# Kernel optimization log

Hardware: AMD Instinct MI355X
Metric: run time of the kernel (lower is better)

## Reference

```python
import jax, jax.numpy as jnp
import numpy as np

B, H, W, C = 8, 64, 64, 64
C8 = C // 8

def setup_inputs() -> dict:
    key = jax.random.key(0)
    ks = jax.random.split(key, 5)
    x = jax.random.normal(ks[0], (B, H, W, C), dtype=jnp.float32)
    # 1x1 conv kernels (fan-in scaled) + biases
    wq = jax.random.normal(ks[1], (C, C8), dtype=jnp.float32) / np.sqrt(C)
    wk = jax.random.normal(ks[2], (C, C8), dtype=jnp.float32) / np.sqrt(C)
    wv = jax.random.normal(ks[3], (C, C), dtype=jnp.float32) / np.sqrt(C)
    bq = jnp.zeros((C8,), dtype=jnp.float32)
    bk = jnp.zeros((C8,), dtype=jnp.float32)
    bv = jnp.zeros((C,), dtype=jnp.float32)
    gamma = jax.random.normal(ks[4], (), dtype=jnp.float32)
    return {"x": x, "wq": wq, "bq": bq, "wk": wk, "bk": bk,
            "wv": wv, "bv": bv, "gamma": gamma}

def reference(x, wq, bq, wk, bk, wv, bv, gamma):
    b, h, w, c = x.shape
    n = h * w
    # 1x1 convs == per-pixel linear projections
    q = (jnp.einsum('bhwc,cd->bhwd', x, wq) + bq).reshape(b, n, -1)  # [B,N,C/8]
    k = (jnp.einsum('bhwc,cd->bhwd', x, wk) + bk).reshape(b, n, -1)  # [B,N,C/8]
    v = (jnp.einsum('bhwc,cd->bhwd', x, wv) + bv).reshape(b, n, -1)  # [B,N,C]
    # Unscaled attention: softmax over keys (last axis), no 1/sqrt(d)
    attn = jax.nn.softmax(jnp.einsum('bnd,bmd->bnm', q, k), axis=-1)  # [B,N,N]
    out = jnp.einsum('bnm,bmc->bnc', attn, v).reshape(b, h, w, c)
    return out * gamma + x
```

## Files before the change

kernel.cpp:

```cpp
#include <hip/hip_runtime.h>
#include <hip/hip_bf16.h>


#define BB 8
#define NN 4096
#define CC 64
#define PSTRIDE 72
#define LOG2E 1.44269504088896f

typedef _Float16 f16;
typedef _Float16 half8 __attribute__((ext_vector_type(8)));
typedef _Float16 half4 __attribute__((ext_vector_type(4)));
typedef __fp16 fp16x2 __attribute__((ext_vector_type(2)));
typedef float floatx4 __attribute__((ext_vector_type(4)));

static __device__ inline half4 pack4(float a, float b, float c, float d) {
    fp16x2 lo = __builtin_amdgcn_cvt_pkrtz(a, b);
    fp16x2 hi = __builtin_amdgcn_cvt_pkrtz(c, d);
    unsigned int lou = __builtin_bit_cast(unsigned int, lo);
    unsigned int hiu = __builtin_bit_cast(unsigned int, hi);
    unsigned long long packed = (unsigned long long)lou | ((unsigned long long)hiu << 32);
    return __builtin_bit_cast(half4, packed);
}


__global__ __launch_bounds__(256) void proj_all_kernel(
    const float* __restrict__ x,
    const float* __restrict__ wq, const float* __restrict__ bq,
    const float* __restrict__ wk, const float* __restrict__ bk,
    const float* __restrict__ wv, const float* __restrict__ bv,
    f16* __restrict__ Qh, f16* __restrict__ Kf, f16* __restrict__ Vf,
    float* __restrict__ qn2, float* __restrict__ kn2)
{
    __shared__ alignas(16) f16 Ws[80][PSTRIDE];
    __shared__ float Bs[80];
    __shared__ alignas(16) f16 Vs[64][68];
    __shared__ alignas(16) f16 Ks[64][12];
    const int tid = threadIdx.x;

    for (int i = tid; i < 4096; i += 256) {
        int cin = i >> 6, cout = i & 63;
        Ws[cout][cin] = (f16)wv[i];
    }
    for (int i = tid; i < 512; i += 256) {
        int cin = i >> 3, c = i & 7;
        Ws[64 + c][cin] = (f16)(wq[i] * LOG2E);
        Ws[72 + c][cin] = (f16)wk[i];
    }
    if (tid < 80)
        Bs[tid] = (tid < 64) ? bv[tid]
                : (tid < 72 ? bq[tid - 64] * LOG2E : bk[tid - 72]);
    __syncthreads();

    const int wave = tid >> 6, lane = tid & 63;
    const int quad = lane >> 4, n16 = lane & 15;
    const long pb = (long)blockIdx.x * 64;
    const long p0 = pb + wave * 16;
    const int  b   = (int)(pb >> 12);
    const int  nnb = (int)(pb & 4095);

    half8 ax[2];
#pragma unroll
    for (int kh = 0; kh < 2; ++kh) {
        const float* xp = x + (p0 + n16) * 64 + kh * 32 + quad * 8;
        float4 x1 = *(const float4*)xp;
        float4 x2 = *(const float4*)(xp + 4);
        ax[kh][0] = (f16)x1.x; ax[kh][1] = (f16)x1.y;
        ax[kh][2] = (f16)x1.z; ax[kh][3] = (f16)x1.w;
        ax[kh][4] = (f16)x2.x; ax[kh][5] = (f16)x2.y;
        ax[kh][6] = (f16)x2.z; ax[kh][7] = (f16)x2.w;
    }

#pragma unroll
    for (int ct = 0; ct < 5; ++ct) {
        const int cout = (ct < 4) ? ct * 16 + n16 : 64 + n16;
        const float bias = Bs[cout];
        half8 b0 = *(const half8*)(&Ws[cout][quad * 8]);
        half8 b1 = *(const half8*)(&Ws[cout][32 + quad * 8]);
        floatx4 acc = {bias, bias, bias, bias};
        acc = __builtin_amdgcn_mfma_f32_16x16x32_f16(ax[0], b0, acc, 0, 0, 0);
        acc = __builtin_amdgcn_mfma_f32_16x16x32_f16(ax[1], b1, acc, 0, 0, 0);
        if (ct < 4) {
#pragma unroll
            for (int r = 0; r < 4; ++r)
                Vs[wave * 16 + quad * 4 + r][ct * 16 + n16] = (f16)acc[r];
        } else {
            float n2[4];
#pragma unroll
            for (int r = 0; r < 4; ++r) n2[r] = acc[r] * acc[r];
#pragma unroll
            for (int d = 1; d < 8; d <<= 1)
#pragma unroll
                for (int r = 0; r < 4; ++r) n2[r] += __shfl_xor(n2[r], d, 64);
            if (n16 == 0) {
#pragma unroll
                for (int r = 0; r < 4; ++r) qn2[p0 + quad * 4 + r] = n2[r];
            } else if (n16 == 8) {
#pragma unroll
                for (int r = 0; r < 4; ++r) kn2[p0 + quad * 4 + r] = n2[r];
            }
            if (n16 < 8) {
                f16* dst = Qh + (p0 + quad * 4) * 8 + n16;
#pragma unroll
                for (int r = 0; r < 4; ++r) dst[r * 8] = (f16)acc[r];
            } else {
#pragma unroll
                for (int r = 0; r < 4; ++r)
                    Ks[wave * 16 + quad * 4 + r][n16 - 8] = (f16)acc[r];
            }
        }
    }
    __syncthreads();

#pragma unroll
    for (int u = 0; u < 2; ++u) {
        const int tt = wave * 2 + u;
        const int kb = tt >> 2, ct = tt & 3;
        half8 v;
#pragma unroll
        for (int j = 0; j < 8; ++j)
            v[j] = Vs[kb * 32 + quad * 8 + j][ct * 16 + n16];
        const size_t kbg = (size_t)b * 128 + (nnb >> 5) + kb;
        *(half8*)(Vf + (kbg * 4 + ct) * 512 + lane * 8) = v;
    }
    if (wave < 2) {
        half8 kp;
#pragma unroll
        for (int e = 0; e < 2; ++e) {
            const int t = wave * 2 + e;
#pragma unroll
            for (int j = 0; j < 4; ++j) {
                f16 v = (f16)0.f;
                if (quad < 2) v = Ks[t * 16 + n16][quad * 4 + j];
                else if (quad == 2 && j == 0) v = (f16)1.f;
                kp[e * 4 + j] = v;
            }
        }
        const size_t kpg = (size_t)b * 128 + (nnb >> 5) + wave;
        *(half8*)(Kf + kpg * 512 + lane * 8) = kp;
    }
}

__global__ __launch_bounds__(256) void knorm_max_kernel(
    const float* __restrict__ kn2, float* __restrict__ Mk2)
{
    __shared__ float red[4];
    const int b = blockIdx.x, tid = threadIdx.x;
    float mx = 0.f;
    for (int i = tid; i < NN; i += 256) mx = fmaxf(mx, kn2[(size_t)b * NN + i]);
#pragma unroll
    for (int d = 1; d < 64; d <<= 1) mx = fmaxf(mx, __shfl_xor(mx, d, 64));
    if ((tid & 63) == 0) red[tid >> 6] = mx;
    __syncthreads();
    if (tid == 0) Mk2[b] = fmaxf(fmaxf(red[0], red[1]), fmaxf(red[2], red[3]));
}

__global__ __launch_bounds__(256, 3) void attn_kernel(
    const f16* __restrict__ Qh, const f16* __restrict__ Kf,
    const f16* __restrict__ Vf,
    const float* __restrict__ qn2, const float* __restrict__ Mk2,
    const float* __restrict__ x, const float* __restrict__ gptr,
    float* __restrict__ out)
{
    __shared__ alignas(16) char smem[24576];
    f16*   Pbuf = (f16*)smem;
    float* Obuf = (float*)smem;
    __shared__ float Ls[4][2][16];

    const int tid  = threadIdx.x;
    const int wave = tid >> 6, lane = tid & 63;
    const int quad = lane >> 4, n16 = lane & 15;
    const int ks = wave;

    const int b  = blockIdx.x & 7;
    const int qt = blockIdx.x >> 3;
    const size_t bN = (size_t)b * NN;

    const float mk2 = Mk2[b];

    half4 bq4[2];
#pragma unroll
    for (int qt2 = 0; qt2 < 2; ++qt2) {
        const int q = qt * 32 + qt2 * 16 + n16;
        const float mf = __builtin_sqrtf(qn2[bN + q] * mk2) - 12.0f;
        half4 v = {0, 0, 0, 0};
        if (quad < 2)
            v = *(const half4*)(Qh + (bN + q) * 8 + quad * 4);
        else if (quad == 2)
            v[0] = (f16)(-mf);
        bq4[qt2] = v;
    }

    floatx4 oacc[2][4];
#pragma unroll
    for (int qt2 = 0; qt2 < 2; ++qt2)
#pragma unroll
        for (int ct = 0; ct < 4; ++ct) oacc[qt2][ct] = (floatx4){0.f, 0.f, 0.f, 0.f};
    float l_loc[2] = {0.f, 0.f};

    const f16* kfb = Kf + ((size_t)b * 128 + ks * 32) * 512;
    const f16* vfb = Vf + ((size_t)b * 128 + ks * 32) * 2048;
    const floatx4 zero4 = {0.f, 0.f, 0.f, 0.f};
    f16* Pw0 = Pbuf + (wave * 2 + 0) * 16 * PSTRIDE;
    f16* Pw1 = Pbuf + (wave * 2 + 1) * 16 * PSTRIDE;

    for (int it = 0; it < 16; ++it) {
        half8 kk0 = *(const half8*)(kfb + (size_t)(it * 2 + 0) * 512 + lane * 8);
        half8 kk1 = *(const half8*)(kfb + (size_t)(it * 2 + 1) * 512 + lane * 8);
        half8 av0[4], av1[4];
#pragma unroll
        for (int ct = 0; ct < 4; ++ct)
            av0[ct] = *(const half8*)(vfb + ((size_t)(it * 2) * 4 + ct) * 512 + lane * 8);
#pragma unroll
        for (int ct = 0; ct < 4; ++ct)
            av1[ct] = *(const half8*)(vfb + ((size_t)(it * 2 + 1) * 4 + ct) * 512 + lane * 8);

        half4 ak[4];
        ak[0] = __builtin_shufflevector(kk0, kk0, 0, 1, 2, 3);
        ak[1] = __builtin_shufflevector(kk0, kk0, 4, 5, 6, 7);
        ak[2] = __builtin_shufflevector(kk1, kk1, 0, 1, 2, 3);
        ak[3] = __builtin_shufflevector(kk1, kk1, 4, 5, 6, 7);

        floatx4 sf[4];
#pragma unroll
        for (int t = 0; t < 4; ++t)
            sf[t] = __builtin_amdgcn_mfma_f32_16x16x16f16(ak[t], bq4[0], zero4, 0, 0, 0);

#pragma unroll
        for (int qt2 = 0; qt2 < 2; ++qt2) {
            if (qt2 == 1) {
#pragma unroll
                for (int t = 0; t < 4; ++t)
                    sf[t] = __builtin_amdgcn_mfma_f32_16x16x16f16(ak[t], bq4[1], zero4, 0, 0, 0);
            }
            float rst[4];
#pragma unroll
            for (int t = 0; t < 4; ++t) {
                float pv0 = __builtin_exp2f(sf[t][0]);
                float pv1 = __builtin_exp2f(sf[t][1]);
                float pv2 = __builtin_exp2f(sf[t][2]);
                float pv3 = __builtin_exp2f(sf[t][3]);
                sf[t][0] = pv0; sf[t][1] = pv1; sf[t][2] = pv2; sf[t][3] = pv3;
                rst[t] = (pv0 + pv1) + (pv2 + pv3);
            }
            l_loc[qt2] += (rst[0] + rst[1]) + (rst[2] + rst[3]);
            f16* Pw = qt2 ? Pw1 : Pw0;
#pragma unroll
            for (int t = 0; t < 4; ++t) {
                half4 pk = pack4(sf[t][0], sf[t][1], sf[t][2], sf[t][3]);
                *(half4*)(Pw + n16 * PSTRIDE + t * 16 + quad * 4) = pk;
            }
        }
        __asm__ volatile("s_waitcnt lgkmcnt(0)" ::: "memory");

#pragma unroll
        for (int qt2 = 0; qt2 < 2; ++qt2) {
            f16* Pw = qt2 ? Pw1 : Pw0;
            half8 bp0 = *(const half8*)(Pw + n16 * PSTRIDE + quad * 8);
            half8 bp1 = *(const half8*)(Pw + n16 * PSTRIDE + 32 + quad * 8);
#pragma unroll
            for (int ct = 0; ct < 4; ++ct)
                oacc[qt2][ct] = __builtin_amdgcn_mfma_f32_16x16x32_f16(av0[ct], bp0, oacc[qt2][ct], 0, 0, 0);
#pragma unroll
            for (int ct = 0; ct < 4; ++ct)
                oacc[qt2][ct] = __builtin_amdgcn_mfma_f32_16x16x32_f16(av1[ct], bp1, oacc[qt2][ct], 0, 0, 0);
        }
    }

    float l_run[2];
#pragma unroll
    for (int qt2 = 0; qt2 < 2; ++qt2) {
        float l = l_loc[qt2];
        l += __shfl_xor(l, 16, 64);
        l += __shfl_xor(l, 32, 64);
        l_run[qt2] = l;
    }

    __syncthreads();
    if (ks > 0) {
#pragma unroll
        for (int qt2 = 0; qt2 < 2; ++qt2) {
            if (quad == 0) Ls[ks][qt2][n16] = l_run[qt2];
            float* ob = Obuf + (((ks - 1) * 2 + qt2) * 64 + lane) * 16;
#pragma unroll
            for (int ct = 0; ct < 4; ++ct)
                *(floatx4*)(ob + ct * 4) = oacc[qt2][ct];
        }
    }
    __syncthreads();
    if (ks == 0) {
        const float g = gptr[0];
#pragma unroll
        for (int qt2 = 0; qt2 < 2; ++qt2) {
            float l = l_run[qt2];
            float o[16];
#pragma unroll
            for (int ct = 0; ct < 4; ++ct)
#pragma unroll
                for (int r = 0; r < 4; ++r) o[ct * 4 + r] = oacc[qt2][ct][r];
#pragma unroll
            for (int p = 1; p < 4; ++p) {
                l += Ls[p][qt2][n16];
                const float* ob = Obuf + (((p - 1) * 2 + qt2) * 64 + lane) * 16;
#pragma unroll
                for (int i = 0; i < 16; ++i) o[i] += ob[i];
            }
            const float scale = g / l;
            const int q = qt * 32 + qt2 * 16 + n16;
#pragma unroll
            for (int ct = 0; ct < 4; ++ct) {
                const size_t idx = (bN + q) * CC + ct * 16 + quad * 4;
                float4 xr = *(const float4*)(x + idx);
                float4 res;
                res.x = o[ct * 4 + 0] * scale + xr.x;
                res.y = o[ct * 4 + 1] * scale + xr.y;
                res.z = o[ct * 4 + 2] * scale + xr.z;
                res.w = o[ct * 4 + 3] * scale + xr.w;
                *(float4*)(out + idx) = res;
            }
        }
    }
}

extern "C" void kernel_launch(void* const* d_in, const int* in_sizes, int n_in,
                              void* d_out, int out_size, void* d_ws, size_t ws_size,
                              hipStream_t stream) {
    const float* x     = (const float*)d_in[0];
    const float* wq    = (const float*)d_in[1];
    const float* bq    = (const float*)d_in[2];
    const float* wk    = (const float*)d_in[3];
    const float* bk    = (const float*)d_in[4];
    const float* wv    = (const float*)d_in[5];
    const float* bv    = (const float*)d_in[6];
    const float* gamma = (const float*)d_in[7];
    float* out = (float*)d_out;

    f16* Qh = (f16*)d_ws;
    f16* Kf = Qh + (size_t)BB * NN * 8;
    f16* Vf = Kf + (size_t)BB * 128 * 512;
    float* qn2 = (float*)(Vf + (size_t)BB * 128 * 4 * 512);
    float* kn2 = qn2 + (size_t)BB * NN;
    float* Mk2 = kn2 + (size_t)BB * NN;

    proj_all_kernel<<<512, 256, 0, stream>>>(x, wq, bq, wk, bk, wv, bv,
                                             Qh, Kf, Vf, qn2, kn2);
    knorm_max_kernel<<<BB, 256, 0, stream>>>(kn2, Mk2);
    attn_kernel<<<BB * 128, 256, 0, stream>>>(Qh, Kf, Vf, qn2, Mk2, x, gamma, out);
}
```

Measured before the change: 128.4 us.

## Software-pipeline attention loop with double-buffered P tiles and K prefetch

The attention loop becomes a software pipeline. Each iteration computes QK^T and exp for step it into one LDS P buffer while running the PV MFMAs for step it-1 from the other buffer, and K and V fragments are prefetched one step ahead. Launch bounds rise to 4 blocks per SM, shared memory grows to 36 KB, and the cross-wave output reduction buffer is padded to stride 20 and read with vector loads to cut bank conflicts. The cost is more LDS and register pressure, which may limit occupancy or force spills.

```diff
diff --git a/kernel.cpp b/kernel.cpp
--- a/kernel.cpp
+++ b/kernel.cpp
@@ -155,17 +155,17 @@
     if (tid == 0) Mk2[b] = fmaxf(fmaxf(red[0], red[1]), fmaxf(red[2], red[3]));
 }
 
-__global__ __launch_bounds__(256, 3) void attn_kernel(
+__global__ __launch_bounds__(256, 4) void attn_kernel(
     const f16* __restrict__ Qh, const f16* __restrict__ Kf,
     const f16* __restrict__ Vf,
     const float* __restrict__ qn2, const float* __restrict__ Mk2,
     const float* __restrict__ x, const float* __restrict__ gptr,
     float* __restrict__ out)
 {
-    __shared__ alignas(16) char smem[24576];
-    f16*   Pbuf = (f16*)smem;
-    float* Obuf = (float*)smem;
+    __shared__ alignas(16) char smem[36864];
     __shared__ float Ls[4][2][16];
+    f16*   Pbase = (f16*)smem;
+    float* Obuf  = (float*)smem;
 
     const int tid  = threadIdx.x;
     const int wave = tid >> 6, lane = tid & 63;
@@ -198,72 +198,136 @@
         for (int ct = 0; ct < 4; ++ct) oacc[qt2][ct] = (floatx4){0.f, 0.f, 0.f, 0.f};
     float l_loc[2] = {0.f, 0.f};
 
-    const f16* kfb = Kf + ((size_t)b * 128 + ks * 32) * 512;
-    const f16* vfb = Vf + ((size_t)b * 128 + ks * 32) * 2048;
+    const f16* kfb = Kf + ((size_t)b * 128 + ks * 32) * 512 + lane * 8;
+    const f16* vfb = Vf + ((size_t)b * 128 + ks * 32) * 2048 + lane * 8;
     const floatx4 zero4 = {0.f, 0.f, 0.f, 0.f};
-    f16* Pw0 = Pbuf + (wave * 2 + 0) * 16 * PSTRIDE;
-    f16* Pw1 = Pbuf + (wave * 2 + 1) * 16 * PSTRIDE;
-
-    for (int it = 0; it < 16; ++it) {
-        half8 kk0 = *(const half8*)(kfb + (size_t)(it * 2 + 0) * 512 + lane * 8);
-        half8 kk1 = *(const half8*)(kfb + (size_t)(it * 2 + 1) * 512 + lane * 8);
-        half8 av0[4], av1[4];
+
+    f16* PA = Pbase + wave * 2304;
+    f16* PB = Pbase + 9216 + wave * 2304;
+
+    half8 kkc0 = *(const half8*)(kfb + 0);
+    half8 kkc1 = *(const half8*)(kfb + 512);
+    half8 kkn0, kkn1;
+    half8 av0[4], av1[4];
+
+    {
+        half4 ak[4];
+        ak[0] = __builtin_shufflevector(kkc0, kkc0, 0, 1, 2, 3);
+        ak[1] = __builtin_shufflevector(kkc0, kkc0, 4, 5, 6, 7);
+        ak[2] = __builtin_shufflevector(kkc1, kkc1, 0, 1, 2, 3);
+        ak[3] = __builtin_shufflevector(kkc1, kkc1, 4, 5, 6, 7);
+
+        kkn0 = *(const half8*)(kfb + 1024);
+        kkn1 = *(const half8*)(kfb + 1536);
 #pragma unroll
         for (int ct = 0; ct < 4; ++ct)
-            av0[ct] = *(const half8*)(vfb + ((size_t)(it * 2) * 4 + ct) * 512 + lane * 8);
+            av0[ct] = *(const half8*)(vfb + (size_t)ct * 512);
 #pragma unroll
         for (int ct = 0; ct < 4; ++ct)
-            av1[ct] = *(const half8*)(vfb + ((size_t)(it * 2 + 1) * 4 + ct) * 512 + lane * 8);
+            av1[ct] = *(const half8*)(vfb + (size_t)(4 + ct) * 512);
+
+        floatx4 sf[4];
+#pragma unroll
+        for (int qt2 = 0; qt2 < 2; ++qt2) {
+#pragma unroll
+            for (int t = 0; t < 4; ++t)
+                sf[t] = __builtin_amdgcn_mfma_f32_16x16x16f16(ak[t], bq4[qt2], zero4, 0, 0, 0);
+            float rst[4];
+            f16* Pw = PA + qt2 * 1152 + n16 * PSTRIDE;
+#pragma unroll
+            for (int t = 0; t < 4; ++t) {
+                float p0 = __builtin_exp2f(sf[t][0]);
+                float p1 = __builtin_exp2f(sf[t][1]);
+                float p2 = __builtin_exp2f(sf[t][2]);
+                float p3 = __builtin_exp2f(sf[t][3]);
+                rst[t] = (p0 + p1) + (p2 + p3);
+                *(half4*)(Pw + t * 16 + quad * 4) = pack4(p0, p1, p2, p3);
+            }
+            l_loc[qt2] += (rst[0] + rst[1]) + (rst[2] + rst[3]);
+        }
+        kkc0 = kkn0; kkc1 = kkn1;
+    }
+
+    for (int it = 1; it < 16; ++it) {
+        f16* Pr = (it & 1) ? PA : PB;
+        f16* Pw = (it & 1) ? PB : PA;
+
+        __asm__ volatile("s_waitcnt lgkmcnt(0)" ::: "memory");
+        half8 bp[2][2];
+#pragma unroll
+        for (int qt2 = 0; qt2 < 2; ++qt2) {
+            const f16* p = Pr + qt2 * 1152 + n16 * PSTRIDE;
+            bp[qt2][0] = *(const half8*)(p + quad * 8);
+            bp[qt2][1] = *(const half8*)(p + 32 + quad * 8);
+        }
 
         half4 ak[4];
-        ak[0] = __builtin_shufflevector(kk0, kk0, 0, 1, 2, 3);
-        ak[1] = __builtin_shufflevector(kk0, kk0, 4, 5, 6, 7);
-        ak[2] = __builtin_shufflevector(kk1, kk1, 0, 1, 2, 3);
-        ak[3] = __builtin_shufflevector(kk1, kk1, 4, 5, 6, 7);
+        ak[0] = __builtin_shufflevector(kkc0, kkc0, 0, 1, 2, 3);
+        ak[1] = __builtin_shufflevector(kkc0, kkc0, 4, 5, 6, 7);
+        ak[2] = __builtin_shufflevector(kkc1, kkc1, 0, 1, 2, 3);
+        ak[3] = __builtin_shufflevector(kkc1, kkc1, 4, 5, 6, 7);
+
+        const int itn = (it < 15) ? it + 1 : 15;
+        kkn0 = *(const half8*)(kfb + (size_t)itn * 1024);
+        kkn1 = *(const half8*)(kfb + (size_t)itn * 1024 + 512);
 
         floatx4 sf[4];
 #pragma unroll
-        for (int t = 0; t < 4; ++t)
-            sf[t] = __builtin_amdgcn_mfma_f32_16x16x16f16(ak[t], bq4[0], zero4, 0, 0, 0);
-
-#pragma unroll
-        for (int qt2 = 0; qt2 < 2; ++qt2) {
-            if (qt2 == 1) {
-#pragma unroll
-                for (int t = 0; t < 4; ++t)
-                    sf[t] = __builtin_amdgcn_mfma_f32_16x16x16f16(ak[t], bq4[1], zero4, 0, 0, 0);
-            }
+        for (int qt2 = 0; qt2 < 2; ++qt2) {
+#pragma unroll
+            for (int t = 0; t < 4; ++t)
+                sf[t] = __builtin_amdgcn_mfma_f32_16x16x16f16(ak[t], bq4[qt2], zero4, 0, 0, 0);
             float rst[4];
+            f16* Pq = Pw + qt2 * 1152 + n16 * PSTRIDE;
 #pragma unroll
             for (int t = 0; t < 4; ++t) {
-                float pv0 = __builtin_exp2f(sf[t][0]);
-                float pv1 = __builtin_exp2f(sf[t][1]);
-                float pv2 = __builtin_exp2f(sf[t][2]);
-                float pv3 = __builtin_exp2f(sf[t][3]);
-                sf[t][0] = pv0; sf[t][1] = pv1; sf[t][2] = pv2; sf[t][3] = pv3;
-                rst[t] = (pv0 + pv1) + (pv2 + pv3);
+                float p0 = __builtin_exp2f(sf[t][0]);
+                float p1 = __builtin_exp2f(sf[t][1]);
+                float p2 = __builtin_exp2f(sf[t][2]);
+                float p3 = __builtin_exp2f(sf[t][3]);
+                rst[t] = (p0 + p1) + (p2 + p3);
+                *(half4*)(Pq + t * 16 + quad * 4) = pack4(p0, p1, p2, p3);
             }
             l_loc[qt2] += (rst[0] + rst[1]) + (rst[2] + rst[3]);
-            f16* Pw = qt2 ? Pw1 : Pw0;
-#pragma unroll
-            for (int t = 0; t < 4; ++t) {
-                half4 pk = pack4(sf[t][0], sf[t][1], sf[t][2], sf[t][3]);
-                *(half4*)(Pw + n16 * PSTRIDE + t * 16 + quad * 4) = pk;
-            }
-        }
+        }
+
+#pragma unroll
+        for (int qt2 = 0; qt2 < 2; ++qt2) {
+#pragma unroll
+            for (int ct = 0; ct < 4; ++ct)
+                oacc[qt2][ct] = __builtin_amdgcn_mfma_f32_16x16x32_f16(av0[ct], bp[qt2][0], oacc[qt2][ct], 0, 0, 0);
+#pragma unroll
+            for (int ct = 0; ct < 4; ++ct)
+                oacc[qt2][ct] = __builtin_amdgcn_mfma_f32_16x16x32_f16(av1[ct], bp[qt2][1], oacc[qt2][ct], 0, 0, 0);
+        }
+
+#pragma unroll
+        for (int ct = 0; ct < 4; ++ct)
+            av0[ct] = *(const half8*)(vfb + ((size_t)(it * 2) * 4 + ct) * 512);
+#pragma unroll
+        for (int ct = 0; ct < 4; ++ct)
+            av1[ct] = *(const half8*)(vfb + ((size_t)(it * 2 + 1) * 4 + ct) * 512);
+
+        kkc0 = kkn0; kkc1 = kkn1;
+    }
+
+    {
         __asm__ volatile("s_waitcnt lgkmcnt(0)" ::: "memory");
-
-#pragma unroll
-        for (int qt2 = 0; qt2 < 2; ++qt2) {
-            f16* Pw = qt2 ? Pw1 : Pw0;
-            half8 bp0 = *(const half8*)(Pw + n16 * PSTRIDE + quad * 8);
-            half8 bp1 = *(const half8*)(Pw + n16 * PSTRIDE + 32 + quad * 8);
-#pragma unroll
-            for (int ct = 0; ct < 4; ++ct)
-                oacc[qt2][ct] = __builtin_amdgcn_mfma_f32_16x16x32_f16(av0[ct], bp0, oacc[qt2][ct], 0, 0, 0);
-#pragma unroll
-            for (int ct = 0; ct < 4; ++ct)
-                oacc[qt2][ct] = __builtin_amdgcn_mfma_f32_16x16x32_f16(av1[ct], bp1, oacc[qt2][ct], 0, 0, 0);
+        half8 bp[2][2];
+#pragma unroll
+        for (int qt2 = 0; qt2 < 2; ++qt2) {
+            const f16* p = PB + qt2 * 1152 + n16 * PSTRIDE;
+            bp[qt2][0] = *(const half8*)(p + quad * 8);
+            bp[qt2][1] = *(const half8*)(p + 32 + quad * 8);
+        }
+#pragma unroll
+        for (int qt2 = 0; qt2 < 2; ++qt2) {
+#pragma unroll
+            for (int ct = 0; ct < 4; ++ct)
+                oacc[qt2][ct] = __builtin_amdgcn_mfma_f32_16x16x32_f16(av0[ct], bp[qt2][0], oacc[qt2][ct], 0, 0, 0);
+#pragma unroll
+            for (int ct = 0; ct < 4; ++ct)
+                oacc[qt2][ct] = __builtin_amdgcn_mfma_f32_16x16x32_f16(av1[ct], bp[qt2][1], oacc[qt2][ct], 0, 0, 0);
         }
     }
 
@@ -281,7 +345,7 @@
 #pragma unroll
         for (int qt2 = 0; qt2 < 2; ++qt2) {
             if (quad == 0) Ls[ks][qt2][n16] = l_run[qt2];
-            float* ob = Obuf + (((ks - 1) * 2 + qt2) * 64 + lane) * 16;
+            float* ob = Obuf + (size_t)(((ks - 1) * 2 + qt2) * 64 + lane) * 20;
 #pragma unroll
             for (int ct = 0; ct < 4; ++ct)
                 *(floatx4*)(ob + ct * 4) = oacc[qt2][ct];
@@ -301,9 +365,13 @@
 #pragma unroll
             for (int p = 1; p < 4; ++p) {
                 l += Ls[p][qt2][n16];
-                const float* ob = Obuf + (((p - 1) * 2 + qt2) * 64 + lane) * 16;
-#pragma unroll
-                for (int i = 0; i < 16; ++i) o[i] += ob[i];
+                const float* ob = Obuf + (size_t)(((p - 1) * 2 + qt2) * 64 + lane) * 20;
+#pragma unroll
+                for (int ct = 0; ct < 4; ++ct) {
+                    floatx4 t = *(const floatx4*)(ob + ct * 4);
+                    o[ct * 4 + 0] += t[0]; o[ct * 4 + 1] += t[1];
+                    o[ct * 4 + 2] += t[2]; o[ct * 4 + 3] += t[3];
+                }
             }
             const float scale = g / l;
             const int q = qt * 32 + qt2 * 16 + n16;
```

Result: no change. 127.4 us (-0.7%).

## Feed P directly from MFMA registers into PV MFMA, removing LDS round-trip

Applied to the files above, without the earlier changes.

The V fragment layout in the prep kernel is permuted so that the score MFMA output (16x16x16, four f16 values per lane) can be packed and fed straight into the P·V MFMA as the B operand, using 16x16x16 instructions instead of 16x16x32. This drops the per-iteration write of P to shared memory, the lgkmcnt wait and the read back. K fragments are also prefetched one iteration ahead. The reduction buffer stride is padded from 16 to 20 floats and read with vector loads to reduce bank conflicts. The cost is twice as many (smaller) MFMA instructions for the P·V product and extra registers for the prefetched K.

```diff
diff --git a/kernel.cpp b/kernel.cpp
--- a/kernel.cpp
+++ b/kernel.cpp
@@ -118,8 +118,11 @@
         const int kb = tt >> 2, ct = tt & 3;
         half8 v;
 #pragma unroll
-        for (int j = 0; j < 8; ++j)
-            v[j] = Vs[kb * 32 + quad * 8 + j][ct * 16 + n16];
+        for (int j = 0; j < 4; ++j)
+            v[j] = Vs[kb * 32 + quad * 4 + j][ct * 16 + n16];
+#pragma unroll
+        for (int j = 0; j < 4; ++j)
+            v[4 + j] = Vs[kb * 32 + 16 + quad * 4 + j][ct * 16 + n16];
         const size_t kbg = (size_t)b * 128 + (nnb >> 5) + kb;
         *(half8*)(Vf + (kbg * 4 + ct) * 512 + lane * 8) = v;
     }
@@ -162,10 +165,9 @@
     const float* __restrict__ x, const float* __restrict__ gptr,
     float* __restrict__ out)
 {
-    __shared__ alignas(16) char smem[24576];
-    f16*   Pbuf = (f16*)smem;
+    __shared__ alignas(16) char smem[30720];
+    __shared__ float Ls[4][2][16];
     float* Obuf = (float*)smem;
-    __shared__ float Ls[4][2][16];
 
     const int tid  = threadIdx.x;
     const int wave = tid >> 6, lane = tid & 63;
@@ -198,72 +200,62 @@
         for (int ct = 0; ct < 4; ++ct) oacc[qt2][ct] = (floatx4){0.f, 0.f, 0.f, 0.f};
     float l_loc[2] = {0.f, 0.f};
 
-    const f16* kfb = Kf + ((size_t)b * 128 + ks * 32) * 512;
-    const f16* vfb = Vf + ((size_t)b * 128 + ks * 32) * 2048;
+    const f16* kfb = Kf + ((size_t)b * 128 + ks * 32) * 512 + lane * 8;
+    const f16* vfb = Vf + ((size_t)b * 128 + ks * 32) * 2048 + lane * 8;
     const floatx4 zero4 = {0.f, 0.f, 0.f, 0.f};
-    f16* Pw0 = Pbuf + (wave * 2 + 0) * 16 * PSTRIDE;
-    f16* Pw1 = Pbuf + (wave * 2 + 1) * 16 * PSTRIDE;
+
+    half8 kkc0 = *(const half8*)(kfb + 0);
+    half8 kkc1 = *(const half8*)(kfb + 512);
 
     for (int it = 0; it < 16; ++it) {
-        half8 kk0 = *(const half8*)(kfb + (size_t)(it * 2 + 0) * 512 + lane * 8);
-        half8 kk1 = *(const half8*)(kfb + (size_t)(it * 2 + 1) * 512 + lane * 8);
-        half8 av0[4], av1[4];
-#pragma unroll
-        for (int ct = 0; ct < 4; ++ct)
-            av0[ct] = *(const half8*)(vfb + ((size_t)(it * 2) * 4 + ct) * 512 + lane * 8);
-#pragma unroll
-        for (int ct = 0; ct < 4; ++ct)
-            av1[ct] = *(const half8*)(vfb + ((size_t)(it * 2 + 1) * 4 + ct) * 512 + lane * 8);
+        half8 avp[2][4];
+#pragma unroll
+        for (int p = 0; p < 2; ++p)
+#pragma unroll
+            for (int ct = 0; ct < 4; ++ct)
+                avp[p][ct] = *(const half8*)(vfb + ((size_t)(it * 2 + p) * 4 + ct) * 512);
 
         half4 ak[4];
-        ak[0] = __builtin_shufflevector(kk0, kk0, 0, 1, 2, 3);
-        ak[1] = __builtin_shufflevector(kk0, kk0, 4, 5, 6, 7);
-        ak[2] = __builtin_shufflevector(kk1, kk1, 0, 1, 2, 3);
-        ak[3] = __builtin_shufflevector(kk1, kk1, 4, 5, 6, 7);
-
-        floatx4 sf[4];
-#pragma unroll
-        for (int t = 0; t < 4; ++t)
-            sf[t] = __builtin_amdgcn_mfma_f32_16x16x16f16(ak[t], bq4[0], zero4, 0, 0, 0);
+        ak[0] = __builtin_shufflevector(kkc0, kkc0, 0, 1, 2, 3);
+        ak[1] = __builtin_shufflevector(kkc0, kkc0, 4, 5, 6, 7);
+        ak[2] = __builtin_shufflevector(kkc1, kkc1, 0, 1, 2, 3);
+        ak[3] = __builtin_shufflevector(kkc1, kkc1, 4, 5, 6, 7);
+
+        const int itn = (it < 15) ? it + 1 : 15;
+        kkc0 = *(const half8*)(kfb + (size_t)itn * 1024);
+        kkc1 = *(const half8*)(kfb + (size_t)itn * 1024 + 512);
 
 #pragma unroll
         for (int qt2 = 0; qt2 < 2; ++qt2) {
-            if (qt2 == 1) {
-#pragma unroll
-                for (int t = 0; t < 4; ++t)
-                    sf[t] = __builtin_amdgcn_mfma_f32_16x16x16f16(ak[t], bq4[1], zero4, 0, 0, 0);
-            }
+            floatx4 sf[4];
+#pragma unroll
+            for (int t = 0; t < 4; ++t)
+                sf[t] = __builtin_amdgcn_mfma_f32_16x16x16f16(ak[t], bq4[qt2], zero4, 0, 0, 0);
+
+            half4 pk[4];
             float rst[4];
 #pragma unroll
             for (int t = 0; t < 4; ++t) {
-                float pv0 = __builtin_exp2f(sf[t][0]);
-                float pv1 = __builtin_exp2f(sf[t][1]);
-                float pv2 = __builtin_exp2f(sf[t][2]);
-                float pv3 = __builtin_exp2f(sf[t][3]);
-                sf[t][0] = pv0; sf[t][1] = pv1; sf[t][2] = pv2; sf[t][3] = pv3;
-                rst[t] = (pv0 + pv1) + (pv2 + pv3);
+                float p0 = __builtin_exp2f(sf[t][0]);
+                float p1 = __builtin_exp2f(sf[t][1]);
+                float p2 = __builtin_exp2f(sf[t][2]);
+                float p3 = __builtin_exp2f(sf[t][3]);
+                rst[t] = (p0 + p1) + (p2 + p3);
+                pk[t] = pack4(p0, p1, p2, p3);
             }
             l_loc[qt2] += (rst[0] + rst[1]) + (rst[2] + rst[3]);
-            f16* Pw = qt2 ? Pw1 : Pw0;
+
 #pragma unroll
             for (int t = 0; t < 4; ++t) {
-                half4 pk = pack4(sf[t][0], sf[t][1], sf[t][2], sf[t][3]);
-                *(half4*)(Pw + n16 * PSTRIDE + t * 16 + quad * 4) = pk;
-            }
-        }
-        __asm__ volatile("s_waitcnt lgkmcnt(0)" ::: "memory");
-
-#pragma unroll
-        for (int qt2 = 0; qt2 < 2; ++qt2) {
-            f16* Pw = qt2 ? Pw1 : Pw0;
-            half8 bp0 = *(const half8*)(Pw + n16 * PSTRIDE + quad * 8);
-            half8 bp1 = *(const half8*)(Pw + n16 * PSTRIDE + 32 + quad * 8);
-#pragma unroll
-            for (int ct = 0; ct < 4; ++ct)
-                oacc[qt2][ct] = __builtin_amdgcn_mfma_f32_16x16x32_f16(av0[ct], bp0, oacc[qt2][ct], 0, 0, 0);
-#pragma unroll
-            for (int ct = 0; ct < 4; ++ct)
-                oacc[qt2][ct] = __builtin_amdgcn_mfma_f32_16x16x32_f16(av1[ct], bp1, oacc[qt2][ct], 0, 0, 0);
+                const int p = t >> 1;
+#pragma unroll
+                for (int ct = 0; ct < 4; ++ct) {
+                    half4 va = (t & 1)
+                        ? __builtin_shufflevector(avp[p][ct], avp[p][ct], 4, 5, 6, 7)
+                        : __builtin_shufflevector(avp[p][ct], avp[p][ct], 0, 1, 2, 3);
+                    oacc[qt2][ct] = __builtin_amdgcn_mfma_f32_16x16x16f16(va, pk[t], oacc[qt2][ct], 0, 0, 0);
+                }
+            }
         }
     }
 
@@ -281,7 +273,7 @@
 #pragma unroll
         for (int qt2 = 0; qt2 < 2; ++qt2) {
             if (quad == 0) Ls[ks][qt2][n16] = l_run[qt2];
-            float* ob = Obuf + (((ks - 1) * 2 + qt2) * 64 + lane) * 16;
+            float* ob = Obuf + (size_t)(((ks - 1) * 2 + qt2) * 64 + lane) * 20;
 #pragma unroll
             for (int ct = 0; ct < 4; ++ct)
                 *(floatx4*)(ob + ct * 4) = oacc[qt2][ct];
@@ -301,9 +293,13 @@
 #pragma unroll
             for (int p = 1; p < 4; ++p) {
                 l += Ls[p][qt2][n16];
-                const float* ob = Obuf + (((p - 1) * 2 + qt2) * 64 + lane) * 16;
-#pragma unroll
-                for (int i = 0; i < 16; ++i) o[i] += ob[i];
+                const float* ob = Obuf + (size_t)(((p - 1) * 2 + qt2) * 64 + lane) * 20;
+#pragma unroll
+                for (int ct = 0; ct < 4; ++ct) {
+                    floatx4 t = *(const floatx4*)(ob + ct * 4);
+                    o[ct * 4 + 0] += t[0]; o[ct * 4 + 1] += t[1];
+                    o[ct * 4 + 2] += t[2]; o[ct * 4 + 3] += t[3];
+                }
             }
             const float scale = g / l;
             const int q = qt * 32 + qt2 * 16 + n16;
```

Result: faster. 123.9 us (-3.5%).
